# Optimization experiments

Measured on AMD Instinct MI355X. Metric: run time of the kernel, lower is better.

Reference implementation:

```python
import jax, jax.numpy as jnp
import numpy as np

B, L, F, A, H = 512, 196, 512, 512, 512  # batch, att locations, feature, att hidden, rnn hidden


def setup_inputs() -> dict:
    key = jax.random.key(0)
    ks = jax.random.split(key, 12)
    s = 0.02
    return {
        "xt": jax.random.normal(ks[0], (B, H), jnp.float32),
        "fc_feats": jax.random.normal(ks[1], (B, F), jnp.float32),
        "att_feats": jax.random.normal(ks[2], (B, L, F), jnp.float32),
        "h0": jax.random.normal(ks[3], (1, B, H), jnp.float32),
        "c0": jax.random.normal(ks[4], (1, B, H), jnp.float32),
        "W_ctx": jax.random.normal(ks[5], (A, F), jnp.float32) * s,
        "b_ctx": jnp.zeros((A,), jnp.float32),
        "W_hid": jax.random.normal(ks[6], (A, H), jnp.float32) * s,
        "b_hid": jnp.zeros((A,), jnp.float32),
        "w_score": jax.random.normal(ks[7], (A,), jnp.float32) * s,
        "b_score": jnp.zeros((), jnp.float32),
        "W_ih": jax.random.normal(ks[8], (4 * H, H + F), jnp.float32) * s,
        "W_hh": jax.random.normal(ks[9], (4 * H, H), jnp.float32) * s,
    }


def reference(xt, fc_feats, att_feats, h0, c0, W_ctx, b_ctx, W_hid, b_hid,
              w_score, b_score, W_ih, W_hh):
    h_prev = h0[-1]  # (B, H)
    c_prev = c0[-1]  # (B, H)
    # Bahdanau additive attention
    img_att = jnp.einsum('blf,af->bla', att_feats, W_ctx) + b_ctx          # (B, L, A)
    hid_att = h_prev @ W_hid.T + b_hid                                     # (B, A)
    alignment = jnp.tanh(img_att + hid_att[:, None, :])                    # (B, L, A)
    scores = jnp.einsum('bla,a->bl', alignment, w_score) + b_score         # (B, L)
    score = jax.nn.softmax(scores, axis=-1)                                # (B, L)
    att_res = jnp.einsum('bl,blf->bf', score, att_feats)                   # (B, F)
    # Single LSTM step, PyTorch gate order (i, f, g, o), no bias
    x = jnp.concatenate([xt, att_res], axis=1)                             # (B, H+F)
    gates = x @ W_ih.T + h_prev @ W_hh.T                                   # (B, 4H)
    i, f, g, o = jnp.split(gates, 4, axis=1)
    i = jax.nn.sigmoid(i)
    f = jax.nn.sigmoid(f)
    g = jnp.tanh(g)
    o = jax.nn.sigmoid(o)
    c = f * c_prev + i * g
    h = o * jnp.tanh(c)
    return h, (h[None], c[None])
```

## Files before the change

### kernel.cpp

```cpp
#include <hip/hip_runtime.h>
#include <stdint.h>

typedef unsigned short u16;
typedef unsigned int   u32;
typedef __attribute__((ext_vector_type(2))) float f32x2;
typedef __attribute__((ext_vector_type(4))) float f32x4;
typedef __attribute__((ext_vector_type(8))) short s16x8;

__device__ __forceinline__ u16 f2bf(float f) {
    u32 x = __float_as_uint(f);
    x += 0x7fffu + ((x >> 16) & 1u);
    return (u16)(x >> 16);
}
__device__ __forceinline__ float tanh_fast(float x) {
    return 1.f - 2.f / (__expf(2.f * x) + 1.f);
}
__device__ __forceinline__ float sigm(float x) {
    return 1.f / (1.f + __expf(-x));
}
__device__ __forceinline__ s16x8 pack8(f32x4 x0, f32x4 x1) {
    union { s16x8 v; u32 w[4]; } r;
    r.w[0] = __builtin_amdgcn_perm(__float_as_uint(x0[1]), __float_as_uint(x0[0]), 0x07060302u);
    r.w[1] = __builtin_amdgcn_perm(__float_as_uint(x0[3]), __float_as_uint(x0[2]), 0x07060302u);
    r.w[2] = __builtin_amdgcn_perm(__float_as_uint(x1[1]), __float_as_uint(x1[0]), 0x07060302u);
    r.w[3] = __builtin_amdgcn_perm(__float_as_uint(x1[3]), __float_as_uint(x1[2]), 0x07060302u);
    return r.v;
}

#define BM 128
#define BN 128
#define BK 64

template<int EPI, bool AF32, bool BF32>
__global__ __launch_bounds__(256) void gemm_bt(
    const void* __restrict__ Ag, const void* __restrict__ B1, const void* __restrict__ B2,
    int lda, int ldb1, int ldb2, int ksplitB, int N, int klen,
    float* __restrict__ outF,
    const float* __restrict__ bias1, const float* __restrict__ bias2,
    const float* __restrict__ hidb, const float* __restrict__ wscore,
    float* __restrict__ scores)
{
    __shared__ __align__(16) u16 As[BM * BK];
    __shared__ __align__(16) u16 Bs[BN * BK];
    const int tid = threadIdx.x;
    const int l   = tid & 63;

    const int nbx = gridDim.x;
    const int nwg = nbx * gridDim.y;
    const int p   = blockIdx.x + blockIdx.y * nbx;
    const int per = nwg >> 3;
    const int lg  = (p & 7) * per + (p >> 3);
    const int n0  = (lg % nbx) * BN;
    const int m0  = (lg / nbx) * BM;

    const int kbeg   = blockIdx.z * klen;
    const int nsteps = klen / BK;
    const int w  = tid >> 6;
    const int wr = (w >> 1) * 64;
    const int wc = (w & 1) * 64;
    const int srow = tid >> 3;
    const int cs   = tid & 7;

    f32x4 acc[4][4] = {};
    f32x4 fa[8], fb[8];
    s16x8 ha[4], hb16[4];

    auto LOAD = [&](int kt) {
        #pragma unroll
        for (int c = 0; c < 4; ++c) {
            int row = c * 32 + srow;
            if constexpr (AF32) {
                const float* ap = (const float*)Ag + (size_t)(m0 + row) * lda + kt + cs * 8;
                fa[2*c]   = *(const f32x4*)ap;
                fa[2*c+1] = *(const f32x4*)(ap + 4);
            } else {
                ha[c] = *(const s16x8*)((const u16*)Ag + (size_t)(m0 + row) * lda + kt + cs * 8);
            }
            int kg = kt + cs * 8;
            if constexpr (BF32) {
                const float* bp = (kg < ksplitB)
                    ? ((const float*)B1 + (size_t)(n0 + row) * ldb1 + kg)
                    : ((const float*)B2 + (size_t)(n0 + row) * ldb2 + (kg - ksplitB));
                fb[2*c]   = *(const f32x4*)bp;
                fb[2*c+1] = *(const f32x4*)(bp + 4);
            } else {
                const u16* bp = (kg < ksplitB)
                    ? ((const u16*)B1 + (size_t)(n0 + row) * ldb1 + kg)
                    : ((const u16*)B2 + (size_t)(n0 + row) * ldb2 + (kg - ksplitB));
                hb16[c] = *(const s16x8*)bp;
            }
        }
    };

    LOAD(kbeg);

    for (int s = 0; s < nsteps; ++s) {
        __syncthreads();
        #pragma unroll
        for (int c = 0; c < 4; ++c) {
            int row = c * 32 + srow;
            int sw = ((cs ^ (row & 7)) * 8);
            s16x8 va, vb;
            if constexpr (AF32) va = pack8(fa[2*c], fa[2*c+1]); else va = ha[c];
            if constexpr (BF32) vb = pack8(fb[2*c], fb[2*c+1]); else vb = hb16[c];
            *(s16x8*)(As + row * BK + sw) = va;
            *(s16x8*)(Bs + row * BK + sw) = vb;
        }
        __syncthreads();
        if (s + 1 < nsteps) LOAD(kbeg + (s + 1) * BK);
        #pragma unroll
        for (int kk = 0; kk < BK; kk += 32) {
            s16x8 af[4], bg[4];
            const int cb = (kk >> 3) + (l >> 4);
            #pragma unroll
            for (int i = 0; i < 4; ++i) {
                int ra = wr + i * 16 + (l & 15);
                af[i] = *(const s16x8*)(As + ra * BK + ((cb ^ (ra & 7)) * 8));
            }
            #pragma unroll
            for (int j = 0; j < 4; ++j) {
                int rb = wc + j * 16 + (l & 15);
                bg[j] = *(const s16x8*)(Bs + rb * BK + ((cb ^ (rb & 7)) * 8));
            }
            #pragma unroll
            for (int i = 0; i < 4; ++i)
                #pragma unroll
                for (int j = 0; j < 4; ++j)
                    acc[i][j] = __builtin_amdgcn_mfma_f32_16x16x32_bf16(af[i], bg[j], acc[i][j], 0, 0, 0);
        }
    }

    const int col0 = l & 15;
    const int rgrp = l >> 4;

    if (EPI == 1) {
        float wsv[4], bs[4]; int gcol[4];
        #pragma unroll
        for (int j = 0; j < 4; ++j) {
            gcol[j] = n0 + wc + j * 16 + col0;
            wsv[j] = wscore[gcol[j]];
            bs[j]  = bias1[gcol[j]] + bias2[gcol[j]];
        }
        #pragma unroll
        for (int i = 0; i < 4; ++i) {
            #pragma unroll
            for (int q = 0; q < 4; ++q) {
                int grow = m0 + wr + i * 16 + rgrp * 4 + q;
                int bb = grow / 196;
                const float* hb = hidb + (size_t)bb * N;
                float s = 0.f;
                #pragma unroll
                for (int j = 0; j < 4; ++j) {
                    float x = acc[i][j][q] + hb[gcol[j]] + bs[j];
                    s += tanh_fast(x) * wsv[j];
                }
                s += __shfl_xor(s, 1);
                s += __shfl_xor(s, 2);
                s += __shfl_xor(s, 4);
                s += __shfl_xor(s, 8);
                if (col0 == 0) atomicAdd(&scores[grow], s);
            }
        }
    } else {
        #pragma unroll
        for (int j = 0; j < 4; ++j) {
            int gcol = n0 + wc + j * 16 + col0;
            #pragma unroll
            for (int i = 0; i < 4; ++i)
                #pragma unroll
                for (int q = 0; q < 4; ++q) {
                    int grow = m0 + wr + i * 16 + rgrp * 4 + q;
                    atomicAdd(&outF[(size_t)grow * N + gcol], acc[i][j][q]);
                }
        }
    }
}

__global__ __launch_bounds__(256) void softmax_attres(
    const float* __restrict__ att, const float* __restrict__ scores,
    const float* __restrict__ xt, const float* __restrict__ h0,
    u16* __restrict__ X)
{
    const int b = blockIdx.x;
    const int tid = threadIdx.x;
    __shared__ float p[200];
    __shared__ float redm[4], reds[4];
    __shared__ float accu[128 * 4];

    float s = (tid < 196) ? scores[b * 196 + tid] : -3.0e38f;
    float m = s;
    #pragma unroll
    for (int d = 32; d; d >>= 1) m = fmaxf(m, __shfl_xor(m, d));
    if ((tid & 63) == 0) redm[tid >> 6] = m;
    __syncthreads();
    m = fmaxf(fmaxf(redm[0], redm[1]), fmaxf(redm[2], redm[3]));

    float e = (tid < 196) ? __expf(s - m) : 0.f;
    float sum = e;
    #pragma unroll
    for (int d = 32; d; d >>= 1) sum += __shfl_xor(sum, d);
    if ((tid & 63) == 0) reds[tid >> 6] = sum;
    __syncthreads();
    sum = reds[0] + reds[1] + reds[2] + reds[3];
    if (tid < 196) p[tid] = e / sum;
    __syncthreads();

    const float* attb = att + (size_t)b * 196 * 512;
    const int half = tid >> 7;
    const int e4   = (tid & 127) * 4;
    f32x4 a = {0.f, 0.f, 0.f, 0.f};
    for (int lq = half; lq < 196; lq += 2) {
        f32x4 u = *(const f32x4*)(attb + (size_t)lq * 512 + e4);
        float pl = p[lq];
        a[0] = fmaf(pl, u[0], a[0]);
        a[1] = fmaf(pl, u[1], a[1]);
        a[2] = fmaf(pl, u[2], a[2]);
        a[3] = fmaf(pl, u[3], a[3]);
    }
    if (half) *(f32x4*)(accu + (tid & 127) * 4) = a;
    __syncthreads();

    u16* Xr = X + (size_t)b * 1536;
    if (!half) {
        f32x4 o = *(const f32x4*)(accu + tid * 4);
        a[0] += o[0]; a[1] += o[1]; a[2] += o[2]; a[3] += o[3];
        ((u32*)(Xr + 512))[tid * 2]     = ((u32)f2bf(a[1]) << 16) | (u32)f2bf(a[0]);
        ((u32*)(Xr + 512))[tid * 2 + 1] = ((u32)f2bf(a[3]) << 16) | (u32)f2bf(a[2]);
    }
    f32x2 xv = ((const f32x2*)(xt + (size_t)b * 512))[tid];
    ((u32*)Xr)[tid] = ((u32)f2bf(xv[1]) << 16) | (u32)f2bf(xv[0]);
    f32x2 hv = ((const f32x2*)(h0 + (size_t)b * 512))[tid];
    ((u32*)(Xr + 1024))[tid] = ((u32)f2bf(hv[1]) << 16) | (u32)f2bf(hv[0]);
}

__global__ __launch_bounds__(256) void lstm_ep(
    const float* __restrict__ gates, const float* __restrict__ c0, float* __restrict__ out)
{
    int idx = blockIdx.x * 256 + threadIdx.x;
    int b = idx >> 9, hh = idx & 511;
    const float* g = gates + ((size_t)b << 11);
    float i_ = sigm(g[hh]);
    float f_ = sigm(g[512 + hh]);
    float g_ = tanh_fast(g[1024 + hh]);
    float o_ = sigm(g[1536 + hh]);
    float c = f_ * c0[idx] + i_ * g_;
    float h = o_ * tanh_fast(c);
    out[idx] = h;
    out[262144 + idx] = h;
    out[524288 + idx] = c;
}

extern "C" void kernel_launch(void* const* d_in, const int* in_sizes, int n_in,
                              void* d_out, int out_size, void* d_ws, size_t ws_size,
                              hipStream_t stream) {
    const float* xt   = (const float*)d_in[0];
    const float* att  = (const float*)d_in[2];
    const float* h0   = (const float*)d_in[3];
    const float* c0   = (const float*)d_in[4];
    const float* Wctx = (const float*)d_in[5];
    const float* bctx = (const float*)d_in[6];
    const float* Whid = (const float*)d_in[7];
    const float* bhid = (const float*)d_in[8];
    const float* wsc  = (const float*)d_in[9];
    const float* Wih  = (const float*)d_in[11];
    const float* Whh  = (const float*)d_in[12];
    float* out = (float*)d_out;

    char* ws = (char*)d_ws;
    float* hidb   = (float*)(ws);
    float* scores = (float*)(ws + 1048576);
    float* gates  = (float*)(ws + 1449984);
    u16*   X      = (u16*)  (ws + 5644288);

    hipMemsetAsync(ws, 0, 5644288, stream);

    gemm_bt<2, true, true><<<dim3(4, 4, 4), 256, 0, stream>>>(
        h0, Whid, Whid, 512, 512, 512, 1 << 28, 512, 128,
        hidb, nullptr, nullptr, nullptr, nullptr, nullptr);

    gemm_bt<1, true, true><<<dim3(4, 784, 1), 256, 0, stream>>>(
        att, Wctx, Wctx, 512, 512, 512, 1 << 28, 512, 512,
        nullptr, bhid, bctx, hidb, wsc, scores);

    softmax_attres<<<512, 256, 0, stream>>>(att, scores, xt, h0, X);

    gemm_bt<2, false, true><<<dim3(16, 4, 4), 256, 0, stream>>>(
        X, Wih, Whh, 1536, 1024, 512, 1024, 2048, 384,
        gates, nullptr, nullptr, nullptr, nullptr, nullptr);

    lstm_ep<<<1024, 256, 0, stream>>>(gates, c0, out);
}
```

Baseline: 511.5 us.

## Stage fp32 tiles via direct global-to-LDS loads with double buffering

The GEMM kernel is rewritten to copy fp32 tiles straight from global memory into LDS with global_load_lds, using two LDS buffers so the next K-slice loads while MFMAs run on the current one. Conversion to bf16 moves to after the LDS read. The activation buffer X is now kept in fp32 so a single fp32 path serves all three GEMMs. This removes the register staging and the extra barrier per step, but doubles LDS bytes per element, halves BK to 32, and doubles the X write traffic.

```diff
diff --git a/kernel.cpp b/kernel.cpp
--- a/kernel.cpp
+++ b/kernel.cpp
@@ -6,6 +6,9 @@
 typedef __attribute__((ext_vector_type(2))) float f32x2;
 typedef __attribute__((ext_vector_type(4))) float f32x4;
 typedef __attribute__((ext_vector_type(8))) short s16x8;
+
+typedef const __attribute__((address_space(1))) void as1_void;
+typedef __attribute__((address_space(3))) void as3_void;
 
 __device__ __forceinline__ u16 f2bf(float f) {
     u32 x = __float_as_uint(f);
@@ -29,21 +32,21 @@
 
 #define BM 128
 #define BN 128
-#define BK 64
-
-template<int EPI, bool AF32, bool BF32>
-__global__ __launch_bounds__(256) void gemm_bt(
-    const void* __restrict__ Ag, const void* __restrict__ B1, const void* __restrict__ B2,
+
+template<int EPI>
+__global__ __launch_bounds__(256) void gemm32(
+    const float* __restrict__ Ag, const float* __restrict__ B1, const float* __restrict__ B2,
     int lda, int ldb1, int ldb2, int ksplitB, int N, int klen,
     float* __restrict__ outF,
     const float* __restrict__ bias1, const float* __restrict__ bias2,
     const float* __restrict__ hidb, const float* __restrict__ wscore,
     float* __restrict__ scores)
 {
-    __shared__ __align__(16) u16 As[BM * BK];
-    __shared__ __align__(16) u16 Bs[BN * BK];
+    __shared__ __align__(16) float As[2][BM * 32];
+    __shared__ __align__(16) float Bs[2][BN * 32];
     const int tid = threadIdx.x;
     const int l   = tid & 63;
+    const int w   = tid >> 6;
 
     const int nbx = gridDim.x;
     const int nwg = nbx * gridDim.y;
@@ -54,80 +57,57 @@
     const int m0  = (lg / nbx) * BM;
 
     const int kbeg   = blockIdx.z * klen;
-    const int nsteps = klen / BK;
-    const int w  = tid >> 6;
+    const int nsteps = klen >> 5;
     const int wr = (w >> 1) * 64;
     const int wc = (w & 1) * 64;
-    const int srow = tid >> 3;
-    const int cs   = tid & 7;
+
+    auto STAGE = [&](int buf, int kt) {
+        #pragma unroll
+        for (int c = 0; c < 4; ++c) {
+            const int slot = c * 256 + tid;
+            const int row  = slot >> 3;
+            const int sch  = (slot & 7) ^ (row & 7);
+            const int wbase = (c * 256 + w * 64) * 4;
+            const float* ga = Ag + (size_t)(m0 + row) * lda + kt + sch * 4;
+            __builtin_amdgcn_global_load_lds((as1_void*)ga, (as3_void*)&As[buf][wbase], 16, 0, 0);
+            const int kg = kt + sch * 4;
+            const float* gb = (kg < ksplitB)
+                ? (B1 + (size_t)(n0 + row) * ldb1 + kg)
+                : (B2 + (size_t)(n0 + row) * ldb2 + (kg - ksplitB));
+            __builtin_amdgcn_global_load_lds((as1_void*)gb, (as3_void*)&Bs[buf][wbase], 16, 0, 0);
+        }
+    };
 
     f32x4 acc[4][4] = {};
-    f32x4 fa[8], fb[8];
-    s16x8 ha[4], hb16[4];
-
-    auto LOAD = [&](int kt) {
-        #pragma unroll
-        for (int c = 0; c < 4; ++c) {
-            int row = c * 32 + srow;
-            if constexpr (AF32) {
-                const float* ap = (const float*)Ag + (size_t)(m0 + row) * lda + kt + cs * 8;
-                fa[2*c]   = *(const f32x4*)ap;
-                fa[2*c+1] = *(const f32x4*)(ap + 4);
-            } else {
-                ha[c] = *(const s16x8*)((const u16*)Ag + (size_t)(m0 + row) * lda + kt + cs * 8);
-            }
-            int kg = kt + cs * 8;
-            if constexpr (BF32) {
-                const float* bp = (kg < ksplitB)
-                    ? ((const float*)B1 + (size_t)(n0 + row) * ldb1 + kg)
-                    : ((const float*)B2 + (size_t)(n0 + row) * ldb2 + (kg - ksplitB));
-                fb[2*c]   = *(const f32x4*)bp;
-                fb[2*c+1] = *(const f32x4*)(bp + 4);
-            } else {
-                const u16* bp = (kg < ksplitB)
-                    ? ((const u16*)B1 + (size_t)(n0 + row) * ldb1 + kg)
-                    : ((const u16*)B2 + (size_t)(n0 + row) * ldb2 + (kg - ksplitB));
-                hb16[c] = *(const s16x8*)bp;
-            }
-        }
-    };
-
-    LOAD(kbeg);
-
+    STAGE(0, kbeg);
+    __syncthreads();
+
+    int cur = 0;
     for (int s = 0; s < nsteps; ++s) {
+        if (s + 1 < nsteps) STAGE(cur ^ 1, kbeg + (s + 1) * 32);
+        s16x8 af[4], bg[4];
+        const int cb = (l >> 4) * 2;
+        #pragma unroll
+        for (int i = 0; i < 4; ++i) {
+            const int row = wr + i * 16 + (l & 15);
+            f32x4 x0 = *(const f32x4*)&As[cur][row * 32 + (cb ^ (row & 7)) * 4];
+            f32x4 x1 = *(const f32x4*)&As[cur][row * 32 + ((cb + 1) ^ (row & 7)) * 4];
+            af[i] = pack8(x0, x1);
+        }
+        #pragma unroll
+        for (int j = 0; j < 4; ++j) {
+            const int row = wc + j * 16 + (l & 15);
+            f32x4 x0 = *(const f32x4*)&Bs[cur][row * 32 + (cb ^ (row & 7)) * 4];
+            f32x4 x1 = *(const f32x4*)&Bs[cur][row * 32 + ((cb + 1) ^ (row & 7)) * 4];
+            bg[j] = pack8(x0, x1);
+        }
+        #pragma unroll
+        for (int i = 0; i < 4; ++i)
+            #pragma unroll
+            for (int j = 0; j < 4; ++j)
+                acc[i][j] = __builtin_amdgcn_mfma_f32_16x16x32_bf16(af[i], bg[j], acc[i][j], 0, 0, 0);
         __syncthreads();
-        #pragma unroll
-        for (int c = 0; c < 4; ++c) {
-            int row = c * 32 + srow;
-            int sw = ((cs ^ (row & 7)) * 8);
-            s16x8 va, vb;
-            if constexpr (AF32) va = pack8(fa[2*c], fa[2*c+1]); else va = ha[c];
-            if constexpr (BF32) vb = pack8(fb[2*c], fb[2*c+1]); else vb = hb16[c];
-            *(s16x8*)(As + row * BK + sw) = va;
-            *(s16x8*)(Bs + row * BK + sw) = vb;
-        }
-        __syncthreads();
-        if (s + 1 < nsteps) LOAD(kbeg + (s + 1) * BK);
-        #pragma unroll
-        for (int kk = 0; kk < BK; kk += 32) {
-            s16x8 af[4], bg[4];
-            const int cb = (kk >> 3) + (l >> 4);
-            #pragma unroll
-            for (int i = 0; i < 4; ++i) {
-                int ra = wr + i * 16 + (l & 15);
-                af[i] = *(const s16x8*)(As + ra * BK + ((cb ^ (ra & 7)) * 8));
-            }
-            #pragma unroll
-            for (int j = 0; j < 4; ++j) {
-                int rb = wc + j * 16 + (l & 15);
-                bg[j] = *(const s16x8*)(Bs + rb * BK + ((cb ^ (rb & 7)) * 8));
-            }
-            #pragma unroll
-            for (int i = 0; i < 4; ++i)
-                #pragma unroll
-                for (int j = 0; j < 4; ++j)
-                    acc[i][j] = __builtin_amdgcn_mfma_f32_16x16x32_bf16(af[i], bg[j], acc[i][j], 0, 0, 0);
-        }
+        cur ^= 1;
     }
 
     const int col0 = l & 15;
@@ -179,7 +159,7 @@
 __global__ __launch_bounds__(256) void softmax_attres(
     const float* __restrict__ att, const float* __restrict__ scores,
     const float* __restrict__ xt, const float* __restrict__ h0,
-    u16* __restrict__ X)
+    float* __restrict__ X)
 {
     const int b = blockIdx.x;
     const int tid = threadIdx.x;
@@ -220,17 +200,16 @@
     if (half) *(f32x4*)(accu + (tid & 127) * 4) = a;
     __syncthreads();
 
-    u16* Xr = X + (size_t)b * 1536;
+    float* Xr = X + (size_t)b * 1536;
     if (!half) {
         f32x4 o = *(const f32x4*)(accu + tid * 4);
         a[0] += o[0]; a[1] += o[1]; a[2] += o[2]; a[3] += o[3];
-        ((u32*)(Xr + 512))[tid * 2]     = ((u32)f2bf(a[1]) << 16) | (u32)f2bf(a[0]);
-        ((u32*)(Xr + 512))[tid * 2 + 1] = ((u32)f2bf(a[3]) << 16) | (u32)f2bf(a[2]);
+        *(f32x4*)(Xr + 512 + e4) = a;
     }
     f32x2 xv = ((const f32x2*)(xt + (size_t)b * 512))[tid];
-    ((u32*)Xr)[tid] = ((u32)f2bf(xv[1]) << 16) | (u32)f2bf(xv[0]);
+    ((f32x2*)Xr)[tid] = xv;
     f32x2 hv = ((const f32x2*)(h0 + (size_t)b * 512))[tid];
-    ((u32*)(Xr + 1024))[tid] = ((u32)f2bf(hv[1]) << 16) | (u32)f2bf(hv[0]);
+    ((f32x2*)(Xr + 1024))[tid] = hv;
 }
 
 __global__ __launch_bounds__(256) void lstm_ep(
@@ -270,21 +249,21 @@
     float* hidb   = (float*)(ws);
     float* scores = (float*)(ws + 1048576);
     float* gates  = (float*)(ws + 1449984);
-    u16*   X      = (u16*)  (ws + 5644288);
+    float* X      = (float*)(ws + 5644288);
 
     hipMemsetAsync(ws, 0, 5644288, stream);
 
-    gemm_bt<2, true, true><<<dim3(4, 4, 4), 256, 0, stream>>>(
+    gemm32<2><<<dim3(4, 4, 4), 256, 0, stream>>>(
         h0, Whid, Whid, 512, 512, 512, 1 << 28, 512, 128,
         hidb, nullptr, nullptr, nullptr, nullptr, nullptr);
 
-    gemm_bt<1, true, true><<<dim3(4, 784, 1), 256, 0, stream>>>(
+    gemm32<1><<<dim3(4, 784, 1), 256, 0, stream>>>(
         att, Wctx, Wctx, 512, 512, 512, 1 << 28, 512, 512,
         nullptr, bhid, bctx, hidb, wsc, scores);
 
     softmax_attres<<<512, 256, 0, stream>>>(att, scores, xt, h0, X);
 
-    gemm_bt<2, false, true><<<dim3(16, 4, 4), 256, 0, stream>>>(
+    gemm32<2><<<dim3(16, 4, 4), 256, 0, stream>>>(
         X, Wih, Whh, 1536, 1024, 512, 1024, 2048, 384,
         gates, nullptr, nullptr, nullptr, nullptr, nullptr);
 
```

New measurement: 529.4 us. 3.5% more time.

## Pre-convert weights to bf16 and stage GEMM tiles via direct global-to-LDS loads

Applied to the files above, without the earlier changes.

Adds a kernel that converts all weight matrices to bf16 once per call, concatenating W_ih and W_hh into one packed matrix. The GEMM now loads A and B tiles straight into shared memory with global_load_lds instead of going through registers. The fp32 A tile (att_feats) is kept in fp32 in LDS and packed to bf16 at fragment read time. This removes the register staging and pack work on the load side. In exchange, the XOR swizzle is dropped, so LDS bank conflicts are likely, and the register prefetch overlap is lost: each step now stages, syncs, computes, then syncs again. LDS use also doubles for the fp32 A path.

```diff
diff --git a/kernel.cpp b/kernel.cpp
--- a/kernel.cpp
+++ b/kernel.cpp
@@ -6,6 +6,9 @@
 typedef __attribute__((ext_vector_type(2))) float f32x2;
 typedef __attribute__((ext_vector_type(4))) float f32x4;
 typedef __attribute__((ext_vector_type(8))) short s16x8;
+
+typedef const __attribute__((address_space(1))) void as1_void;
+typedef __attribute__((address_space(3))) void as3_void;
 
 __device__ __forceinline__ u16 f2bf(float f) {
     u32 x = __float_as_uint(f);
@@ -31,19 +34,21 @@
 #define BN 128
 #define BK 64
 
-template<int EPI, bool AF32, bool BF32>
-__global__ __launch_bounds__(256) void gemm_bt(
-    const void* __restrict__ Ag, const void* __restrict__ B1, const void* __restrict__ B2,
-    int lda, int ldb1, int ldb2, int ksplitB, int N, int klen,
+template<int EPI, bool AF32>
+__global__ __launch_bounds__(256) void gemm(
+    const void* __restrict__ Ag, const u16* __restrict__ Bg,
+    int lda, int ldb, int N, int klen,
     float* __restrict__ outF,
     const float* __restrict__ bias1, const float* __restrict__ bias2,
     const float* __restrict__ hidb, const float* __restrict__ wscore,
     float* __restrict__ scores)
 {
-    __shared__ __align__(16) u16 As[BM * BK];
-    __shared__ __align__(16) u16 Bs[BN * BK];
+    constexpr int ABYTES = AF32 ? (BM * BK * 4) : (BM * BK * 2);
+    __shared__ __align__(16) char Abuf[ABYTES];
+    __shared__ __align__(16) u16 Bsb[BN * BK];
     const int tid = threadIdx.x;
     const int l   = tid & 63;
+    const int w   = tid >> 6;
 
     const int nbx = gridDim.x;
     const int nwg = nbx * gridDim.y;
@@ -55,72 +60,62 @@
 
     const int kbeg   = blockIdx.z * klen;
     const int nsteps = klen / BK;
-    const int w  = tid >> 6;
     const int wr = (w >> 1) * 64;
     const int wc = (w & 1) * 64;
-    const int srow = tid >> 3;
-    const int cs   = tid & 7;
+
+    auto STAGE = [&](int kt) {
+        if constexpr (AF32) {
+            #pragma unroll
+            for (int c = 0; c < 8; ++c) {
+                const int slot = c * 256 + tid;
+                const int row = slot >> 4, ch = slot & 15;
+                const float* ga = (const float*)Ag + (size_t)(m0 + row) * lda + kt + ch * 4;
+                __builtin_amdgcn_global_load_lds((as1_void*)ga,
+                    (as3_void*)(Abuf + (c * 256 + w * 64) * 16), 16, 0, 0);
+            }
+        } else {
+            #pragma unroll
+            for (int c = 0; c < 4; ++c) {
+                const int slot = c * 256 + tid;
+                const int row = slot >> 3, ch = slot & 7;
+                const u16* ga = (const u16*)Ag + (size_t)(m0 + row) * lda + kt + ch * 8;
+                __builtin_amdgcn_global_load_lds((as1_void*)ga,
+                    (as3_void*)(Abuf + (c * 256 + w * 64) * 16), 16, 0, 0);
+            }
+        }
+        #pragma unroll
+        for (int c = 0; c < 4; ++c) {
+            const int slot = c * 256 + tid;
+            const int row = slot >> 3, ch = slot & 7;
+            const u16* gb = Bg + (size_t)(n0 + row) * ldb + kt + ch * 8;
+            __builtin_amdgcn_global_load_lds((as1_void*)gb,
+                (as3_void*)((char*)Bsb + (c * 256 + w * 64) * 16), 16, 0, 0);
+        }
+    };
 
     f32x4 acc[4][4] = {};
-    f32x4 fa[8], fb[8];
-    s16x8 ha[4], hb16[4];
-
-    auto LOAD = [&](int kt) {
-        #pragma unroll
-        for (int c = 0; c < 4; ++c) {
-            int row = c * 32 + srow;
-            if constexpr (AF32) {
-                const float* ap = (const float*)Ag + (size_t)(m0 + row) * lda + kt + cs * 8;
-                fa[2*c]   = *(const f32x4*)ap;
-                fa[2*c+1] = *(const f32x4*)(ap + 4);
-            } else {
-                ha[c] = *(const s16x8*)((const u16*)Ag + (size_t)(m0 + row) * lda + kt + cs * 8);
-            }
-            int kg = kt + cs * 8;
-            if constexpr (BF32) {
-                const float* bp = (kg < ksplitB)
-                    ? ((const float*)B1 + (size_t)(n0 + row) * ldb1 + kg)
-                    : ((const float*)B2 + (size_t)(n0 + row) * ldb2 + (kg - ksplitB));
-                fb[2*c]   = *(const f32x4*)bp;
-                fb[2*c+1] = *(const f32x4*)(bp + 4);
-            } else {
-                const u16* bp = (kg < ksplitB)
-                    ? ((const u16*)B1 + (size_t)(n0 + row) * ldb1 + kg)
-                    : ((const u16*)B2 + (size_t)(n0 + row) * ldb2 + (kg - ksplitB));
-                hb16[c] = *(const s16x8*)bp;
-            }
-        }
-    };
-
-    LOAD(kbeg);
+    const int k0 = (l >> 4) * 8;
 
     for (int s = 0; s < nsteps; ++s) {
+        STAGE(kbeg + s * BK);
         __syncthreads();
-        #pragma unroll
-        for (int c = 0; c < 4; ++c) {
-            int row = c * 32 + srow;
-            int sw = ((cs ^ (row & 7)) * 8);
-            s16x8 va, vb;
-            if constexpr (AF32) va = pack8(fa[2*c], fa[2*c+1]); else va = ha[c];
-            if constexpr (BF32) vb = pack8(fb[2*c], fb[2*c+1]); else vb = hb16[c];
-            *(s16x8*)(As + row * BK + sw) = va;
-            *(s16x8*)(Bs + row * BK + sw) = vb;
-        }
-        __syncthreads();
-        if (s + 1 < nsteps) LOAD(kbeg + (s + 1) * BK);
         #pragma unroll
         for (int kk = 0; kk < BK; kk += 32) {
             s16x8 af[4], bg[4];
-            const int cb = (kk >> 3) + (l >> 4);
             #pragma unroll
             for (int i = 0; i < 4; ++i) {
-                int ra = wr + i * 16 + (l & 15);
-                af[i] = *(const s16x8*)(As + ra * BK + ((cb ^ (ra & 7)) * 8));
+                const int row = wr + i * 16 + (l & 15);
+                if constexpr (AF32) {
+                    const float* ap = (const float*)Abuf + row * BK + kk + k0;
+                    af[i] = pack8(*(const f32x4*)ap, *(const f32x4*)(ap + 4));
+                } else {
+                    af[i] = *(const s16x8*)((const u16*)Abuf + row * BK + kk + k0);
+                }
             }
             #pragma unroll
             for (int j = 0; j < 4; ++j) {
-                int rb = wc + j * 16 + (l & 15);
-                bg[j] = *(const s16x8*)(Bs + rb * BK + ((cb ^ (rb & 7)) * 8));
+                const int row = wc + j * 16 + (l & 15);
+                bg[j] = *(const s16x8*)(Bsb + row * BK + kk + k0);
             }
             #pragma unroll
             for (int i = 0; i < 4; ++i)
@@ -128,6 +123,7 @@
                 for (int j = 0; j < 4; ++j)
                     acc[i][j] = __builtin_amdgcn_mfma_f32_16x16x32_bf16(af[i], bg[j], acc[i][j], 0, 0, 0);
         }
+        __syncthreads();
     }
 
     const int col0 = l & 15;
@@ -176,6 +172,33 @@
     }
 }
 
+__global__ __launch_bounds__(256) void cvt_w(
+    const float* __restrict__ Wctx, const float* __restrict__ Whid,
+    const float* __restrict__ Wih,  const float* __restrict__ Whh,
+    u16* __restrict__ Wctxb, u16* __restrict__ Whidb, u16* __restrict__ Wgb)
+{
+    const int gid = blockIdx.x * 256 + threadIdx.x;
+    const float* src;
+    u16* dst;
+    if (gid < 32768) {
+        src = Wctx + (size_t)gid * 8;
+        dst = Wctxb + (size_t)gid * 8;
+    } else if (gid < 65536) {
+        src = Whid + (size_t)(gid - 32768) * 8;
+        dst = Whidb + (size_t)(gid - 32768) * 8;
+    } else {
+        const int g2 = gid - 65536;
+        const int n  = g2 / 192;
+        const int k8 = (g2 - n * 192) * 8;
+        dst = Wgb + (size_t)n * 1536 + k8;
+        src = (k8 < 1024) ? (Wih + (size_t)n * 1024 + k8)
+                          : (Whh + (size_t)n * 512 + (k8 - 1024));
+    }
+    f32x4 x0 = *(const f32x4*)src;
+    f32x4 x1 = *(const f32x4*)(src + 4);
+    *(s16x8*)dst = pack8(x0, x1);
+}
+
 __global__ __launch_bounds__(256) void softmax_attres(
     const float* __restrict__ att, const float* __restrict__ scores,
     const float* __restrict__ xt, const float* __restrict__ h0,
@@ -224,8 +247,8 @@
     if (!half) {
         f32x4 o = *(const f32x4*)(accu + tid * 4);
         a[0] += o[0]; a[1] += o[1]; a[2] += o[2]; a[3] += o[3];
-        ((u32*)(Xr + 512))[tid * 2]     = ((u32)f2bf(a[1]) << 16) | (u32)f2bf(a[0]);
-        ((u32*)(Xr + 512))[tid * 2 + 1] = ((u32)f2bf(a[3]) << 16) | (u32)f2bf(a[2]);
+        ((u32*)(Xr + 512 + e4))[0] = ((u32)f2bf(a[1]) << 16) | (u32)f2bf(a[0]);
+        ((u32*)(Xr + 512 + e4))[1] = ((u32)f2bf(a[3]) << 16) | (u32)f2bf(a[2]);
     }
     f32x2 xv = ((const f32x2*)(xt + (size_t)b * 512))[tid];
     ((u32*)Xr)[tid] = ((u32)f2bf(xv[1]) << 16) | (u32)f2bf(xv[0]);
@@ -270,22 +293,27 @@
     float* hidb   = (float*)(ws);
     float* scores = (float*)(ws + 1048576);
     float* gates  = (float*)(ws + 1449984);
-    u16*   X      = (u16*)  (ws + 5644288);
+    u16*   Xb     = (u16*)  (ws + 5644288);
+    u16*   Wctxb  = (u16*)  (ws + 7217152);
+    u16*   Whidb  = (u16*)  (ws + 7741440);
+    u16*   Wgb    = (u16*)  (ws + 8265728);
 
     hipMemsetAsync(ws, 0, 5644288, stream);
 
-    gemm_bt<2, true, true><<<dim3(4, 4, 4), 256, 0, stream>>>(
-        h0, Whid, Whid, 512, 512, 512, 1 << 28, 512, 128,
+    cvt_w<<<1792, 256, 0, stream>>>(Wctx, Whid, Wih, Whh, Wctxb, Whidb, Wgb);
+
+    gemm<2, true><<<dim3(4, 4, 4), 256, 0, stream>>>(
+        h0, Whidb, 512, 512, 512, 128,
         hidb, nullptr, nullptr, nullptr, nullptr, nullptr);
 
-    gemm_bt<1, true, true><<<dim3(4, 784, 1), 256, 0, stream>>>(
-        att, Wctx, Wctx, 512, 512, 512, 1 << 28, 512, 512,
+    gemm<1, true><<<dim3(4, 784, 1), 256, 0, stream>>>(
+        att, Wctxb, 512, 512, 512, 512,
         nullptr, bhid, bctx, hidb, wsc, scores);
 
-    softmax_attres<<<512, 256, 0, stream>>>(att, scores, xt, h0, X);
-
-    gemm_bt<2, false, true><<<dim3(16, 4, 4), 256, 0, stream>>>(
-        X, Wih, Whh, 1536, 1024, 512, 1024, 2048, 384,
+    softmax_attres<<<512, 256, 0, stream>>>(att, scores, xt, h0, Xb);
+
+    gemm<2, false><<<dim3(16, 4, 4), 256, 0, stream>>>(
+        Xb, Wgb, 1536, 1536, 2048, 384,
         gates, nullptr, nullptr, nullptr, nullptr, nullptr);
 
     lstm_ep<<<1024, 256, 0, stream>>>(gates, c0, out);
```

New measurement: 498.6 us. -2.5%, faster.
